# Optimization experiments

Measured on AMD Instinct MI355X. Metric: run time of the kernel, lower is better.

Reference implementation:

```python
import jax, jax.numpy as jnp
import numpy as np

BANDLIMIT = 0.5
STEP_SCALE = 1.0  # refiner default step_scale_value
LN_EPS = 1e-5


def _layernorm(x, g, b):
    mu = jnp.mean(x, axis=-1, keepdims=True)
    xc = x - mu
    inv = jax.lax.rsqrt(jnp.mean(xc * xc, axis=-1, keepdims=True) + LN_EPS)
    return xc * inv * g + b


def setup_inputs() -> dict:
    key = jax.random.key(0)
    ks = jax.random.split(key, 12)
    B, C, H, W = 16, 384, 64, 64
    P = 192  # conj-sym half of state_dim=384
    x = jax.random.normal(ks[0], (B, C, H, W), dtype=jnp.float32)
    ln1_g = 1.0 + 0.1 * jax.random.normal(ks[1], (C,), dtype=jnp.float32)
    ln1_b = 0.1 * jax.random.normal(ks[2], (C,), dtype=jnp.float32)
    # stable diagonal A: negative real part, HiPPO-like imaginary ladder
    lam_re = -(0.3 + jax.random.uniform(ks[3], (P,), dtype=jnp.float32))
    lam_im = jnp.pi * jnp.arange(P, dtype=jnp.float32)
    Lambda = jnp.stack([lam_re, lam_im], axis=-1)          # [P,2] (re,im)
    Bmat = jax.random.normal(ks[4], (P, C, 2), dtype=jnp.float32) / np.sqrt(C)
    Cmat = jax.random.normal(ks[5], (C, P, 2), dtype=jnp.float32) / np.sqrt(P)
    D = jax.random.normal(ks[6], (C,), dtype=jnp.float32)
    log_step = jax.random.uniform(ks[7], (P,), dtype=jnp.float32,
                                  minval=float(np.log(1e-3)), maxval=float(np.log(0.1)))
    ln2_g = 1.0 + 0.1 * jax.random.normal(ks[8], (C,), dtype=jnp.float32)
    ln2_b = 0.1 * jax.random.normal(ks[9], (C,), dtype=jnp.float32)
    W_enc = jax.random.normal(ks[10], (2 * C, C), dtype=jnp.float32) / np.sqrt(C)
    W_dec = jax.random.normal(ks[11], (C, C), dtype=jnp.float32) / np.sqrt(C)
    return {"x": x, "ln1_g": ln1_g, "ln1_b": ln1_b, "Lambda": Lambda,
            "Bmat": Bmat, "Cmat": Cmat, "D": D, "log_step": log_step,
            "ln2_g": ln2_g, "ln2_b": ln2_b, "W_enc": W_enc, "W_dec": W_dec}


def reference(x, ln1_g, ln1_b, Lambda, Bmat, Cmat, D, log_step, ln2_g, ln2_b, W_enc, W_dec):
    Bsz, C, H, W = x.shape
    u = x.reshape(Bsz, C, H * W).transpose(0, 2, 1)        # [B, L, C]

    # --- S5Block: attn branch ---
    fx = _layernorm(u, ln1_g, ln1_b)
    res = fx

    lam = Lambda[..., 0] + 1j * Lambda[..., 1]             # [P] complex
    Bc = Bmat[..., 0] + 1j * Bmat[..., 1]                  # [P, C]
    Cc = Cmat[..., 0] + 1j * Cmat[..., 1]                  # [C, P]
    step = STEP_SCALE * jnp.exp(log_step)                  # [P]
    # bandlimit mask on C (as in S5 with bandlimit=0.5)
    freqs = (step / STEP_SCALE) * jnp.abs(Lambda[..., 1]) / (2.0 * jnp.pi)
    mask = (freqs < BANDLIMIT * 0.5).astype(Cc.dtype)
    Cc = Cc * mask
    # ZOH discretization
    lam_bar = jnp.exp(lam * step)                          # [P]
    B_bar = ((lam_bar - 1.0) / lam)[:, None] * Bc          # [P, C]
    Bu = jnp.einsum('ph,blh->blp', B_bar, fx.astype(B_bar.dtype))  # [B,L,P] complex
    lam_el = jnp.broadcast_to(lam_bar, Bu.shape)

    def binop(a, b):
        # linear recurrence composition: x <- a2*(a1*x + b1) + b2
        return a[0] * b[0], b[0] * a[1] + b[1]

    _, xs = jax.lax.associative_scan(binop, (lam_el, Bu), axis=1)  # [B,L,P]
    y = 2.0 * jnp.real(jnp.einsum('hp,blp->blh', Cc, xs)) + D * fx
    y = jax.nn.gelu(y, approximate=False) + res

    # --- S5Block: GEGLU FFN branch ---
    fy = _layernorm(y, ln2_g, ln2_b)
    z = fy @ W_enc.T                                       # [B,L,2C]
    z1, z2 = jnp.split(z, 2, axis=-1)
    z = z1 * jax.nn.gelu(z2, approximate=False)
    y = z @ W_dec.T + fy

    return y.transpose(0, 2, 1).reshape(Bsz, C, H, W)
```

## Files before the change

### kernel.cpp

```cpp
#include <hip/hip_runtime.h>
#include <hip/hip_bf16.h>
#include <math.h>

typedef __attribute__((ext_vector_type(4))) float f32x4;
typedef __attribute__((ext_vector_type(8))) short s16x8;
typedef unsigned short u16;
typedef unsigned int u32;

#define CDIM 384
#define PDIM 192
#define LDIM 4096
#define BSZ  16
#define MDIM 65536
#define KD   384
#define BM 128
#define BN 128
#define BK 32

__device__ __forceinline__ u16 f2bf(float f) {
    u32 x = __float_as_uint(f);
    x += 0x7fffu + ((x >> 16) & 1u);
    return (u16)(x >> 16);
}
__device__ __forceinline__ float bf2f(u16 v) {
    return __uint_as_float(((u32)v) << 16);
}
__device__ __forceinline__ float gelu_exact(float x) {
    return 0.5f * x * (1.0f + erff(x * 0.7071067811865476f));
}
__device__ __forceinline__ float gelu_fast(float x) {
    float w = -1.5957691216f * x * (1.0f + 0.044715f * x * x);
    return x / (1.0f + __expf(w));
}
__device__ __forceinline__ void gld_lds16(const u16* g, u16* l) {
    __builtin_amdgcn_global_load_lds(
        (const __attribute__((address_space(1))) void*)g,
        (__attribute__((address_space(3))) void*)l, 16, 0, 0);
}

__global__ __launch_bounds__(256) void k_setup(
    const float* __restrict__ Lambda, const float* __restrict__ Bmat,
    const float* __restrict__ Cmat, const float* __restrict__ log_step,
    const float* __restrict__ W_enc, const float* __restrict__ W_dec,
    u16* __restrict__ Wb, u16* __restrict__ Wc, u16* __restrict__ We,
    u16* __restrict__ Wd, float* __restrict__ lam_bar)
{
    int idx = blockIdx.x * 256 + threadIdx.x;
    if (idx < 73728) {
        int p = idx / CDIM, c = idx % CDIM;
        float st  = expf(log_step[p]);
        float lre = Lambda[2*p], lim = Lambda[2*p+1];
        float el  = expf(lre * st);
        float lbr = el * cosf(lim * st);
        float lbi = el * sinf(lim * st);
        float dd  = lre*lre + lim*lim;
        float a = lbr - 1.0f, b = lbi;
        float cr = (a * lre + b * lim) / dd;
        float ci = (b * lre - a * lim) / dd;
        float Br = Bmat[2*(p*CDIM + c)], Bi = Bmat[2*(p*CDIM + c) + 1];
        Wb[p*KD + c]          = f2bf(cr*Br - ci*Bi);
        Wb[(PDIM + p)*KD + c] = f2bf(cr*Bi + ci*Br);
    } else if (idx < 147456) {
        int e = idx - 73728;
        int h = e / PDIM, p = e % PDIM;
        float st  = expf(log_step[p]);
        float lim = Lambda[2*p+1];
        float freq = st * fabsf(lim) / 6.283185307179586f;
        float sc = (freq < 0.25f) ? 2.0f : 0.0f;
        Wc[h*KD + p]        = f2bf( sc * Cmat[2*(h*PDIM + p)]);
        Wc[h*KD + PDIM + p] = f2bf(-sc * Cmat[2*(h*PDIM + p) + 1]);
    } else if (idx < 442368) {
        int e = idx - 147456;
        We[e] = f2bf(W_enc[e]);
    } else if (idx < 589824) {
        int e = idx - 442368;
        Wd[e] = f2bf(W_dec[e]);
    } else if (idx < 590016) {
        int p = idx - 589824;
        float st  = expf(log_step[p]);
        float lre = Lambda[2*p], lim = Lambda[2*p+1];
        float el  = expf(lre * st);
        lam_bar[2*p]   = el * cosf(lim * st);
        lam_bar[2*p+1] = el * sinf(lim * st);
    }
}

__global__ __launch_bounds__(256) void k_ln1(
    const float* __restrict__ x, const float* __restrict__ g,
    const float* __restrict__ bb, u16* __restrict__ fx)
{
    __shared__ float tile[CDIM * 36];
    __shared__ float mu_sh[32], inv_sh[32];
    int b  = blockIdx.x >> 7;
    int l0 = (blockIdx.x & 127) * 32;
    int tid = threadIdx.x;
    const float* src = x + ((size_t)b * CDIM) * LDIM + l0;
    #pragma unroll
    for (int it = 0; it < 12; it++) {
        int s = it * 256 + tid;
        int ch = s >> 3, c4 = (s & 7) * 4;
        float4 v = *(const float4*)(src + (size_t)ch * LDIM + c4);
        *(float4*)(tile + ch * 36 + c4) = v;
    }
    __syncthreads();
    int j = tid >> 3, k = tid & 7;
    float sum = 0.f, sq = 0.f;
    for (int c = k; c < CDIM; c += 8) {
        float v = tile[c * 36 + j];
        sum += v; sq += v * v;
    }
    sum += __shfl_xor(sum, 1); sq += __shfl_xor(sq, 1);
    sum += __shfl_xor(sum, 2); sq += __shfl_xor(sq, 2);
    sum += __shfl_xor(sum, 4); sq += __shfl_xor(sq, 4);
    float mu  = sum * (1.0f / CDIM);
    float var = sq * (1.0f / CDIM) - mu * mu;
    float inv = rsqrtf(var + 1e-5f);
    if (k == 0) { mu_sh[j] = mu; inv_sh[j] = inv; }
    __syncthreads();
    u16* dst = fx + ((size_t)(b * LDIM + l0)) * CDIM;
    #pragma unroll
    for (int it = 0; it < 12; it++) {
        int s  = it * 256 + tid;
        int cq = s % 96, jj = s / 96;
        int c  = cq * 4;
        float m2 = mu_sh[jj], iv = inv_sh[jj];
        float4 gv = *(const float4*)(g + c);
        float4 bv = *(const float4*)(bb + c);
        ushort4 o;
        o.x = f2bf((tile[(c+0)*36 + jj] - m2) * iv * gv.x + bv.x);
        o.y = f2bf((tile[(c+1)*36 + jj] - m2) * iv * gv.y + bv.y);
        o.z = f2bf((tile[(c+2)*36 + jj] - m2) * iv * gv.z + bv.z);
        o.w = f2bf((tile[(c+3)*36 + jj] - m2) * iv * gv.w + bv.w);
        *(ushort4*)(dst + (size_t)jj * CDIM + c) = o;
    }
}

template<bool SWAP>
__device__ __forceinline__ void gemm_core(
    const u16* __restrict__ A, int lda, const u16* __restrict__ Bw,
    int m0, int n0, u16* a_sh, u16* b_sh, f32x4 acc[4][4])
{
    const int tid  = threadIdx.x;
    const int w    = tid >> 6, lane = tid & 63;
    const int t16  = lane & 15, quad = lane >> 4;
    const int wm   = w >> 1,   wn   = w & 1;
    const int lr  = lane >> 2;
    const int cbg = (lane & 3) ^ ((lane >> 3) & 3);
    const u16* gA0 = A  + (size_t)(m0 + w*32 + lr) * lda + cbg*8;
    const u16* gA1 = gA0 + (size_t)16 * lda;
    const u16* gB0 = Bw + (size_t)(n0 + w*32 + lr) * KD + cbg*8;
    const u16* gB1 = gB0 + (size_t)16 * KD;
    u16* lA0 = a_sh + (w*32) * BK;
    u16* lA1 = lA0 + 16*BK;
    u16* lB0 = b_sh + (w*32) * BK;
    u16* lB1 = lB0 + 16*BK;
    const int pos = (quad ^ ((t16 >> 1) & 3)) * 8;
    const u16* ard = a_sh + (wm*64 + t16) * BK + pos;
    const u16* brd = b_sh + (wn*64 + t16) * BK + pos;
    #pragma unroll
    for (int i = 0; i < 4; i++)
        #pragma unroll
        for (int j = 0; j < 4; j++) acc[i][j] = (f32x4){0.f,0.f,0.f,0.f};
    for (int kb = 0; kb < KD; kb += BK) {
        __syncthreads();
        gld_lds16(gA0 + kb, lA0);
        gld_lds16(gA1 + kb, lA1);
        gld_lds16(gB0 + kb, lB0);
        gld_lds16(gB1 + kb, lB1);
        __syncthreads();
        s16x8 af[4], bfr[4];
        #pragma unroll
        for (int i = 0; i < 4; i++) af[i]  = *(const s16x8*)(ard + i*16*BK);
        #pragma unroll
        for (int j = 0; j < 4; j++) bfr[j] = *(const s16x8*)(brd + j*16*BK);
        #pragma unroll
        for (int i = 0; i < 4; i++)
            #pragma unroll
            for (int j = 0; j < 4; j++) {
                if (SWAP)
                    acc[i][j] = __builtin_amdgcn_mfma_f32_16x16x32_bf16(bfr[j], af[i], acc[i][j], 0,0,0);
                else
                    acc[i][j] = __builtin_amdgcn_mfma_f32_16x16x32_bf16(af[i], bfr[j], acc[i][j], 0,0,0);
            }
    }
}

__global__ __launch_bounds__(256) void k_gemm_bu(
    const u16* __restrict__ fx, const u16* __restrict__ Wb, u16* __restrict__ Bu)
{
    __shared__ __align__(16) u16 a_sh[BM*BK], b_sh[BN*BK];
    int m0 = blockIdx.x * BM, n0 = blockIdx.y * BN;
    f32x4 acc[4][4];
    gemm_core<false>(fx, CDIM, Wb, m0, n0, a_sh, b_sh, acc);
    int lane = threadIdx.x & 63, w = threadIdx.x >> 6;
    int t16 = lane & 15, quad = lane >> 4, wm = w >> 1, wn = w & 1;
    #pragma unroll
    for (int i = 0; i < 4; i++)
        #pragma unroll
        for (int j = 0; j < 4; j++)
            #pragma unroll
            for (int rr = 0; rr < 4; rr++) {
                int m = m0 + wm*64 + i*16 + quad*4 + rr;
                int n = n0 + wn*64 + j*16 + t16;
                Bu[(size_t)m * CDIM + n] = f2bf(acc[i][j][rr]);
            }
}

__global__ __launch_bounds__(256) void k_gemm_y(
    const u16* __restrict__ xs, const u16* __restrict__ Wc,
    const u16* __restrict__ fx, const float* __restrict__ Dv, u16* __restrict__ y)
{
    __shared__ __align__(16) u16 a_sh[BM*BK], b_sh[BN*BK];
    int m0 = blockIdx.x * BM, n0 = blockIdx.y * BN;
    f32x4 acc[4][4];
    gemm_core<false>(xs, CDIM, Wc, m0, n0, a_sh, b_sh, acc);
    int lane = threadIdx.x & 63, w = threadIdx.x >> 6;
    int t16 = lane & 15, quad = lane >> 4, wm = w >> 1, wn = w & 1;
    float dv[4];
    #pragma unroll
    for (int j = 0; j < 4; j++) dv[j] = Dv[n0 + wn*64 + j*16 + t16];
    #pragma unroll
    for (int i = 0; i < 4; i++)
        #pragma unroll
        for (int j = 0; j < 4; j++)
            #pragma unroll
            for (int rr = 0; rr < 4; rr++) {
                int m = m0 + wm*64 + i*16 + quad*4 + rr;
                int n = n0 + wn*64 + j*16 + t16;
                float fxv = bf2f(fx[(size_t)m * CDIM + n]);
                float v = acc[i][j][rr] + dv[j] * fxv;
                y[(size_t)m * CDIM + n] = f2bf(gelu_fast(v) + fxv);
            }
}

__global__ __launch_bounds__(256) void k_gemm_zg(
    const u16* __restrict__ fy, const u16* __restrict__ We, u16* __restrict__ zg)
{
    __shared__ __align__(16) u16 sh[8448];
    u16* a_sh = sh;
    u16* b_sh = sh + BM*BK;
    const int tid = threadIdx.x;
    const int w = tid >> 6, lane = tid & 63;
    const int t16 = lane & 15, quad = lane >> 4;
    const int wm = w >> 1, wn = w & 1;
    const int m0 = blockIdx.x * BM;
    const int c0 = blockIdx.y * 64;
    const int lr  = lane >> 2;
    const int cbg = (lane & 3) ^ ((lane >> 3) & 3);
    const u16* gA0 = fy + (size_t)(m0 + w*32 + lr) * CDIM + cbg*8;
    const u16* gA1 = gA0 + (size_t)16 * CDIM;
    int brow = c0 + w*32 + ((w >= 2) ? 320 : 0);
    const u16* gB0 = We + (size_t)(brow + lr) * KD + cbg*8;
    const u16* gB1 = gB0 + (size_t)16 * KD;
    u16* lA0 = a_sh + (w*32) * BK;
    u16* lA1 = lA0 + 16*BK;
    u16* lB0 = b_sh + (w*32) * BK;
    u16* lB1 = lB0 + 16*BK;
    const int pos = (quad ^ ((t16 >> 1) & 3)) * 8;
    const u16* ard = a_sh + (wm*64 + t16) * BK + pos;
    const u16* brd = b_sh + (wn*64 + t16) * BK + pos;
    f32x4 acc[4][4];
    #pragma unroll
    for (int i = 0; i < 4; i++)
        #pragma unroll
        for (int j = 0; j < 4; j++) acc[i][j] = (f32x4){0.f,0.f,0.f,0.f};
    for (int kb = 0; kb < KD; kb += BK) {
        __syncthreads();
        gld_lds16(gA0 + kb, lA0);
        gld_lds16(gA1 + kb, lA1);
        gld_lds16(gB0 + kb, lB0);
        gld_lds16(gB1 + kb, lB1);
        __syncthreads();
        s16x8 af[4], bfr[4];
        #pragma unroll
        for (int i = 0; i < 4; i++) af[i]  = *(const s16x8*)(ard + i*16*BK);
        #pragma unroll
        for (int j = 0; j < 4; j++) bfr[j] = *(const s16x8*)(brd + j*16*BK);
        #pragma unroll
        for (int i = 0; i < 4; i++)
            #pragma unroll
            for (int j = 0; j < 4; j++)
                acc[i][j] = __builtin_amdgcn_mfma_f32_16x16x32_bf16(af[i], bfr[j], acc[i][j], 0,0,0);
    }
    __syncthreads();
    if (wn == 1) {
        #pragma unroll
        for (int i = 0; i < 4; i++)
            #pragma unroll
            for (int j = 0; j < 4; j++)
                #pragma unroll
                for (int rr = 0; rr < 4; rr++) {
                    int m = wm*64 + i*16 + quad*4 + rr;
                    int c = j*16 + t16;
                    sh[m*66 + c] = f2bf(gelu_fast(acc[i][j][rr]));
                }
    }
    __syncthreads();
    if (wn == 0) {
        #pragma unroll
        for (int i = 0; i < 4; i++)
            #pragma unroll
            for (int j = 0; j < 4; j++)
                #pragma unroll
                for (int rr = 0; rr < 4; rr++) {
                    int m = wm*64 + i*16 + quad*4 + rr;
                    int c = j*16 + t16;
                    float gv = bf2f(sh[m*66 + c]);
                    zg[(size_t)(m0 + m) * CDIM + c0 + c] = f2bf(acc[i][j][rr] * gv);
                }
    }
}

__global__ __launch_bounds__(256) void k_gemm_out(
    const u16* __restrict__ zg, const u16* __restrict__ Wd,
    const u16* __restrict__ fy, float* __restrict__ out)
{
    __shared__ __align__(16) u16 a_sh[BM*BK], b_sh[BN*BK];
    int m0 = blockIdx.x * BM, n0 = blockIdx.y * BN;
    f32x4 acc[4][4];
    gemm_core<true>(zg, CDIM, Wd, m0, n0, a_sh, b_sh, acc);
    int lane = threadIdx.x & 63, w = threadIdx.x >> 6;
    int t16 = lane & 15, quad = lane >> 4, wm = w >> 1, wn = w & 1;
    int b = m0 >> 12;
    #pragma unroll
    for (int i = 0; i < 4; i++)
        #pragma unroll
        for (int j = 0; j < 4; j++)
            #pragma unroll
            for (int rr = 0; rr < 4; rr++) {
                int nn = n0 + wn*64 + j*16 + quad*4 + rr;
                int mm = m0 + wm*64 + i*16 + t16;
                float fyv = bf2f(fy[(size_t)mm * CDIM + nn]);
                int l = mm & 4095;
                out[((size_t)(b * CDIM + nn)) * LDIM + l] = acc[i][j][rr] + fyv;
            }
}

__global__ __launch_bounds__(192) void k_scan_a(
    const u16* __restrict__ Bu, const float* __restrict__ lam_bar,
    float* __restrict__ summ)
{
    int b = blockIdx.x >> 6, ch = blockIdx.x & 63;
    int p = threadIdx.x;
    float lr = lam_bar[2*p], li = lam_bar[2*p+1];
    float xr = 0.f, xi = 0.f;
    const u16* base = Bu + (size_t)(b * LDIM + ch * 64) * CDIM;
    #pragma unroll 8
    for (int i = 0; i < 64; i++) {
        float br = bf2f(base[(size_t)i * CDIM + p]);
        float bi = bf2f(base[(size_t)i * CDIM + PDIM + p]);
        float nr = lr * xr - li * xi + br;
        float ni = lr * xi + li * xr + bi;
        xr = nr; xi = ni;
    }
    size_t o = (size_t)(b * 64 + ch) * CDIM + p;
    summ[o] = xr;
    summ[o + PDIM] = xi;
}

__global__ __launch_bounds__(256) void k_scan_b(
    const float* __restrict__ lam_bar, float* __restrict__ summ)
{
    int id = blockIdx.x * 256 + threadIdx.x;
    if (id >= BSZ * PDIM) return;
    int b = id / PDIM, p = id % PDIM;
    float ar = lam_bar[2*p], ai = lam_bar[2*p+1];
    #pragma unroll
    for (int s = 0; s < 6; s++) {
        float nr = ar * ar - ai * ai, ni = 2.f * ar * ai;
        ar = nr; ai = ni;
    }
    float cr = 0.f, ci = 0.f;
    #pragma unroll 4
    for (int ch = 0; ch < 64; ch++) {
        size_t o = (size_t)(b * 64 + ch) * CDIM + p;
        float sr = summ[o], si = summ[o + PDIM];
        summ[o] = cr; summ[o + PDIM] = ci;
        float nr = ar * cr - ai * ci + sr;
        float ni = ar * ci + ai * cr + si;
        cr = nr; ci = ni;
    }
}

__global__ __launch_bounds__(192) void k_scan_c(
    u16* __restrict__ Bu, const float* __restrict__ lam_bar,
    const float* __restrict__ summ)
{
    int b = blockIdx.x >> 6, ch = blockIdx.x & 63;
    int p = threadIdx.x;
    float lr = lam_bar[2*p], li = lam_bar[2*p+1];
    size_t oc = (size_t)(b * 64 + ch) * CDIM + p;
    float xr = summ[oc], xi = summ[oc + PDIM];
    u16* base = Bu + (size_t)(b * LDIM + ch * 64) * CDIM;
    #pragma unroll 8
    for (int i = 0; i < 64; i++) {
        float br = bf2f(base[(size_t)i * CDIM + p]);
        float bi = bf2f(base[(size_t)i * CDIM + PDIM + p]);
        float nr = lr * xr - li * xi + br;
        float ni = lr * xi + li * xr + bi;
        xr = nr; xi = ni;
        base[(size_t)i * CDIM + p] = f2bf(xr);
        base[(size_t)i * CDIM + PDIM + p] = f2bf(xi);
    }
}

__global__ __launch_bounds__(256) void k_ln2(
    const u16* __restrict__ y, const float* __restrict__ g,
    const float* __restrict__ bb, u16* __restrict__ fy)
{
    int w = threadIdx.x >> 6, lane = threadIdx.x & 63;
    size_t m = (size_t)blockIdx.x * 4 + w;
    const u16* row = y + m * CDIM;
    float v[6];
    float sum = 0.f, sq = 0.f;
    #pragma unroll
    for (int i = 0; i < 6; i++) {
        v[i] = bf2f(row[lane + 64 * i]);
        sum += v[i]; sq += v[i] * v[i];
    }
    #pragma unroll
    for (int o = 1; o < 64; o <<= 1) {
        sum += __shfl_xor(sum, o); sq += __shfl_xor(sq, o);
    }
    float mu  = sum * (1.0f / CDIM);
    float var = sq * (1.0f / CDIM) - mu * mu;
    float inv = rsqrtf(var + 1e-5f);
    u16* dst = fy + m * CDIM;
    #pragma unroll
    for (int i = 0; i < 6; i++) {
        int c = lane + 64 * i;
        dst[c] = f2bf((v[i] - mu) * inv * g[c] + bb[c]);
    }
}

extern "C" void kernel_launch(void* const* d_in, const int* in_sizes, int n_in,
                              void* d_out, int out_size, void* d_ws, size_t ws_size,
                              hipStream_t stream)
{
    const float* x        = (const float*)d_in[0];
    const float* ln1_g    = (const float*)d_in[1];
    const float* ln1_b    = (const float*)d_in[2];
    const float* Lambda   = (const float*)d_in[3];
    const float* Bmat     = (const float*)d_in[4];
    const float* Cmat     = (const float*)d_in[5];
    const float* Dvec     = (const float*)d_in[6];
    const float* log_step = (const float*)d_in[7];
    const float* ln2_g    = (const float*)d_in[8];
    const float* ln2_b    = (const float*)d_in[9];
    const float* W_enc    = (const float*)d_in[10];
    const float* W_dec    = (const float*)d_in[11];

    char* ws = (char*)d_ws;
    const size_t HBF = (size_t)MDIM * CDIM * 2;
    u16* fx = (u16*)(ws);
    u16* fy = (u16*)(ws + HBF);
    u16* bu = (u16*)(ws + 2 * HBF);
    u16* zg = (u16*)(ws + 2 * HBF);
    char* wbase = ws + 3 * HBF;
    u16* Wb = (u16*)(wbase);
    u16* Wc = (u16*)(wbase + 294912);
    u16* We = (u16*)(wbase + 589824);
    u16* Wd = (u16*)(wbase + 1179648);
    float* lam_bar = (float*)(wbase + 1474560);
    float* summ    = (float*)(wbase + 1476096);
    u16* yb  = (u16*)d_out;
    float* out = (float*)d_out;

    k_setup<<<2305, 256, 0, stream>>>(Lambda, Bmat, Cmat, log_step, W_enc, W_dec,
                                      Wb, Wc, We, Wd, lam_bar);
    k_ln1<<<2048, 256, 0, stream>>>(x, ln1_g, ln1_b, fx);
    k_gemm_bu<<<dim3(512, 3), 256, 0, stream>>>(fx, Wb, bu);
    k_scan_a<<<1024, 192, 0, stream>>>(bu, lam_bar, summ);
    k_scan_b<<<12, 256, 0, stream>>>(lam_bar, summ);
    k_scan_c<<<1024, 192, 0, stream>>>(bu, lam_bar, summ);
    k_gemm_y<<<dim3(512, 3), 256, 0, stream>>>(bu, Wc, fx, Dvec, yb);
    k_ln2<<<16384, 256, 0, stream>>>(yb, ln2_g, ln2_b, fy);
    k_gemm_zg<<<dim3(512, 6), 256, 0, stream>>>(fy, We, zg);
    k_gemm_out<<<dim3(512, 3), 256, 0, stream>>>(zg, Wd, fy, out);
}
```

Baseline: 472.2 us.

## Double-buffer GEMM LDS tiles and remap blocks with XCD-aware swizzle

Each GEMM main loop now uses two LDS buffers: the tile for step k+1 is fetched with global_load_lds while MFMAs run on tile k, which drops one barrier per iteration. Block indices are also remapped so that consecutive workgroups, which are spread round-robin across the 8 XCDs, land on neighbouring tiles and share L2 reuse. In exchange LDS use per block doubles, which may lower occupancy. Correctness depends on the single barrier being enough, since the async LDS writes for the next tile must have landed before that tile is read.

```diff
diff --git a/kernel.cpp b/kernel.cpp
--- a/kernel.cpp
+++ b/kernel.cpp
@@ -16,6 +16,7 @@
 #define BM 128
 #define BN 128
 #define BK 32
+#define NT (KD / BK)
 
 __device__ __forceinline__ u16 f2bf(float f) {
     u32 x = __float_as_uint(f);
@@ -36,6 +37,15 @@
     __builtin_amdgcn_global_load_lds(
         (const __attribute__((address_space(1))) void*)g,
         (__attribute__((address_space(3))) void*)l, 16, 0, 0);
+}
+
+__device__ __forceinline__ void swz_decode(int NY, int& mt, int& nt) {
+    int bid = blockIdx.x + gridDim.x * blockIdx.y;
+    int nwg = gridDim.x * gridDim.y;
+    int cpx = nwg >> 3;
+    int work = (bid & 7) * cpx + (bid >> 3);
+    mt = work / NY;
+    nt = work - mt * NY;
 }
 
 __global__ __launch_bounds__(256) void k_setup(
@@ -161,18 +171,29 @@
     for (int i = 0; i < 4; i++)
         #pragma unroll
         for (int j = 0; j < 4; j++) acc[i][j] = (f32x4){0.f,0.f,0.f,0.f};
-    for (int kb = 0; kb < KD; kb += BK) {
+    gld_lds16(gA0, lA0);
+    gld_lds16(gA1, lA1);
+    gld_lds16(gB0, lB0);
+    gld_lds16(gB1, lB1);
+    int cur = 0;
+    #pragma unroll 2
+    for (int t = 0; t < NT; ++t) {
         __syncthreads();
-        gld_lds16(gA0 + kb, lA0);
-        gld_lds16(gA1 + kb, lA1);
-        gld_lds16(gB0 + kb, lB0);
-        gld_lds16(gB1 + kb, lB1);
-        __syncthreads();
+        if (t + 1 < NT) {
+            int kb = (t + 1) * BK;
+            int nxt = cur ^ 1;
+            gld_lds16(gA0 + kb, lA0 + nxt * (BM*BK));
+            gld_lds16(gA1 + kb, lA1 + nxt * (BM*BK));
+            gld_lds16(gB0 + kb, lB0 + nxt * (BN*BK));
+            gld_lds16(gB1 + kb, lB1 + nxt * (BN*BK));
+        }
+        const u16* ac = ard + cur * (BM*BK);
+        const u16* bc = brd + cur * (BN*BK);
         s16x8 af[4], bfr[4];
         #pragma unroll
-        for (int i = 0; i < 4; i++) af[i]  = *(const s16x8*)(ard + i*16*BK);
-        #pragma unroll
-        for (int j = 0; j < 4; j++) bfr[j] = *(const s16x8*)(brd + j*16*BK);
+        for (int i = 0; i < 4; i++) af[i]  = *(const s16x8*)(ac + i*16*BK);
+        #pragma unroll
+        for (int j = 0; j < 4; j++) bfr[j] = *(const s16x8*)(bc + j*16*BK);
         #pragma unroll
         for (int i = 0; i < 4; i++)
             #pragma unroll
@@ -182,14 +203,17 @@
                 else
                     acc[i][j] = __builtin_amdgcn_mfma_f32_16x16x32_bf16(af[i], bfr[j], acc[i][j], 0,0,0);
             }
+        cur ^= 1;
     }
 }
 
 __global__ __launch_bounds__(256) void k_gemm_bu(
     const u16* __restrict__ fx, const u16* __restrict__ Wb, u16* __restrict__ Bu)
 {
-    __shared__ __align__(16) u16 a_sh[BM*BK], b_sh[BN*BK];
-    int m0 = blockIdx.x * BM, n0 = blockIdx.y * BN;
+    __shared__ __align__(16) u16 a_sh[2*BM*BK], b_sh[2*BN*BK];
+    int mt, nt;
+    swz_decode(gridDim.y, mt, nt);
+    int m0 = mt * BM, n0 = nt * BN;
     f32x4 acc[4][4];
     gemm_core<false>(fx, CDIM, Wb, m0, n0, a_sh, b_sh, acc);
     int lane = threadIdx.x & 63, w = threadIdx.x >> 6;
@@ -210,8 +234,10 @@
     const u16* __restrict__ xs, const u16* __restrict__ Wc,
     const u16* __restrict__ fx, const float* __restrict__ Dv, u16* __restrict__ y)
 {
-    __shared__ __align__(16) u16 a_sh[BM*BK], b_sh[BN*BK];
-    int m0 = blockIdx.x * BM, n0 = blockIdx.y * BN;
+    __shared__ __align__(16) u16 a_sh[2*BM*BK], b_sh[2*BN*BK];
+    int mt, nt;
+    swz_decode(gridDim.y, mt, nt);
+    int m0 = mt * BM, n0 = nt * BN;
     f32x4 acc[4][4];
     gemm_core<false>(xs, CDIM, Wc, m0, n0, a_sh, b_sh, acc);
     int lane = threadIdx.x & 63, w = threadIdx.x >> 6;
@@ -236,15 +262,17 @@
 __global__ __launch_bounds__(256) void k_gemm_zg(
     const u16* __restrict__ fy, const u16* __restrict__ We, u16* __restrict__ zg)
 {
-    __shared__ __align__(16) u16 sh[8448];
+    __shared__ __align__(16) u16 sh[4*BM*BK];
     u16* a_sh = sh;
-    u16* b_sh = sh + BM*BK;
+    u16* b_sh = sh + 2*BM*BK;
     const int tid = threadIdx.x;
     const int w = tid >> 6, lane = tid & 63;
     const int t16 = lane & 15, quad = lane >> 4;
     const int wm = w >> 1, wn = w & 1;
-    const int m0 = blockIdx.x * BM;
-    const int c0 = blockIdx.y * 64;
+    int mt, nt;
+    swz_decode(gridDim.y, mt, nt);
+    const int m0 = mt * BM;
+    const int c0 = nt * 64;
     const int lr  = lane >> 2;
     const int cbg = (lane & 3) ^ ((lane >> 3) & 3);
     const u16* gA0 = fy + (size_t)(m0 + w*32 + lr) * CDIM + cbg*8;
@@ -264,23 +292,35 @@
     for (int i = 0; i < 4; i++)
         #pragma unroll
         for (int j = 0; j < 4; j++) acc[i][j] = (f32x4){0.f,0.f,0.f,0.f};
-    for (int kb = 0; kb < KD; kb += BK) {
+    gld_lds16(gA0, lA0);
+    gld_lds16(gA1, lA1);
+    gld_lds16(gB0, lB0);
+    gld_lds16(gB1, lB1);
+    int cur = 0;
+    #pragma unroll 2
+    for (int t = 0; t < NT; ++t) {
         __syncthreads();
-        gld_lds16(gA0 + kb, lA0);
-        gld_lds16(gA1 + kb, lA1);
-        gld_lds16(gB0 + kb, lB0);
-        gld_lds16(gB1 + kb, lB1);
-        __syncthreads();
+        if (t + 1 < NT) {
+            int kb = (t + 1) * BK;
+            int nxt = cur ^ 1;
+            gld_lds16(gA0 + kb, lA0 + nxt * (BM*BK));
+            gld_lds16(gA1 + kb, lA1 + nxt * (BM*BK));
+            gld_lds16(gB0 + kb, lB0 + nxt * (BN*BK));
+            gld_lds16(gB1 + kb, lB1 + nxt * (BN*BK));
+        }
+        const u16* ac = ard + cur * (BM*BK);
+        const u16* bc = brd + cur * (BN*BK);
         s16x8 af[4], bfr[4];
         #pragma unroll
-        for (int i = 0; i < 4; i++) af[i]  = *(const s16x8*)(ard + i*16*BK);
-        #pragma unroll
-        for (int j = 0; j < 4; j++) bfr[j] = *(const s16x8*)(brd + j*16*BK);
+        for (int i = 0; i < 4; i++) af[i]  = *(const s16x8*)(ac + i*16*BK);
+        #pragma unroll
+        for (int j = 0; j < 4; j++) bfr[j] = *(const s16x8*)(bc + j*16*BK);
         #pragma unroll
         for (int i = 0; i < 4; i++)
             #pragma unroll
             for (int j = 0; j < 4; j++)
                 acc[i][j] = __builtin_amdgcn_mfma_f32_16x16x32_bf16(af[i], bfr[j], acc[i][j], 0,0,0);
+        cur ^= 1;
     }
     __syncthreads();
     if (wn == 1) {
@@ -315,8 +355,10 @@
     const u16* __restrict__ zg, const u16* __restrict__ Wd,
     const u16* __restrict__ fy, float* __restrict__ out)
 {
-    __shared__ __align__(16) u16 a_sh[BM*BK], b_sh[BN*BK];
-    int m0 = blockIdx.x * BM, n0 = blockIdx.y * BN;
+    __shared__ __align__(16) u16 a_sh[2*BM*BK], b_sh[2*BN*BK];
+    int mt, nt;
+    swz_decode(gridDim.y, mt, nt);
+    int m0 = mt * BM, n0 = nt * BN;
     f32x4 acc[4][4];
     gemm_core<true>(zg, CDIM, Wd, m0, n0, a_sh, b_sh, acc);
     int lane = threadIdx.x & 63, w = threadIdx.x >> 6;
```

Result: faster. 447.0 us (-5.3%).
